# Kernel optimization log

Hardware: AMD Instinct MI355X
Metric: run time of the kernel (lower is better)

The kernel has to match this reference:

```python
import jax, jax.numpy as jnp
import numpy as np

B, T, D = 8, 1024, 512
V = 8192  # codebook_size


def setup_inputs() -> dict:
    key = jax.random.key(0)
    k1, k2, k3 = jax.random.split(key, 3)
    scale_w = float(np.sqrt(2.0 / (D + V)))  # xavier_uniform-ish scale
    scale_c = float(np.sqrt(2.0 / (V + D)))
    return {
        "inputs": jax.random.normal(k1, (B, T, D), dtype=jnp.float32),
        "codebook": jax.random.normal(k2, (V, D), dtype=jnp.float32) * scale_c,
        "W_logits": jax.random.normal(k3, (V, D), dtype=jnp.float32) * scale_w,
        "b_logits": jnp.zeros((V,), dtype=jnp.float32),
    }


def reference(inputs, codebook, W_logits, b_logits):
    # logits = Linear(input_dim -> codebook_size)
    logits = jnp.einsum("btd,vd->btv", inputs, W_logits) + b_logits  # [B,T,V]
    # eval mode: no gumbel noise, no temperature division
    soft_tokens = jax.nn.softmax(logits, axis=-1)
    token_indices = jnp.argmax(soft_tokens, axis=-1)  # [B,T]
    hard_tokens = jax.nn.one_hot(token_indices, codebook.shape[0], dtype=soft_tokens.dtype)
    # straight-through: hard values, soft gradients
    tokens_for_lookup = soft_tokens + jax.lax.stop_gradient(hard_tokens - soft_tokens)
    quantized = jnp.einsum("btv,vd->btd", tokens_for_lookup, codebook)  # [B,T,D]
    commitment_loss = jnp.mean((quantized - jax.lax.stop_gradient(inputs)) ** 2)
    return quantized, token_indices, commitment_loss, soft_tokens, logits
```

## Files before the change

kernel.cpp:

```cpp
#include <hip/hip_runtime.h>
#include <hip/hip_bf16.h>

#define BT_ 8192
#define D_  512
#define V_  8192

#define OFF_Q      0
#define OFF_TOK    4194304
#define OFF_LOSS   4202496
#define OFF_SOFT   4202497
#define OFF_LOGITS 71311361
#define STAGE_F    62922752

#define TAU  0.02f
#define EXP_NEG_TAU 0.98019867f
#define MAXC 64

typedef __attribute__((ext_vector_type(8))) short bf16x8;
typedef __attribute__((ext_vector_type(4))) float f32x4;
typedef __attribute__((ext_vector_type(4))) unsigned short u16x4;

__device__ __forceinline__ unsigned short bf16rne(float f) {
  unsigned int u = __float_as_uint(f);
  return (unsigned short)((u + 0x7fffu + ((u >> 16) & 1u)) >> 16);
}

__global__ __launch_bounds__(256) void to_bf16_k(const f32x4* __restrict__ x,
                                                 const f32x4* __restrict__ w,
                                                 u16x4* __restrict__ xa,
                                                 u16x4* __restrict__ wb) {
  const int n4 = (BT_ * D_) / 4;
  const int half = gridDim.x >> 1;
  const bool isw = blockIdx.x >= half;
  const f32x4* __restrict__ s = isw ? w : x;
  u16x4* __restrict__ d = isw ? wb : xa;
  const int b0 = isw ? blockIdx.x - half : blockIdx.x;
  for (int i = b0 * 256 + threadIdx.x; i < n4; i += half * 256) {
    const f32x4 v = s[i];
    u16x4 o;
    o[0] = bf16rne(v[0]); o[1] = bf16rne(v[1]);
    o[2] = bf16rne(v[2]); o[3] = bf16rne(v[3]);
    d[i] = o;
  }
}

__device__ __forceinline__ void gload_lds16(const void* g, void* l) {
  __builtin_amdgcn_global_load_lds((const __attribute__((address_space(1))) void*)g,
                                   (__attribute__((address_space(3))) void*)l,
                                   16, 0, 0);
}

__device__ __forceinline__ void barf() {
  __builtin_amdgcn_s_barrier();
  asm volatile("" ::: "memory");
}
__device__ __forceinline__ void vmcnt2() { asm volatile("s_waitcnt vmcnt(2)" ::: "memory"); }
__device__ __forceinline__ void vmcnt0() { asm volatile("s_waitcnt vmcnt(0)" ::: "memory"); }

__device__ __forceinline__ void stage_unit(const char* __restrict__ tb, char* ldsRegion,
                                           int ktile, int half, int wid, int lane) {
#pragma unroll
  for (int issue = 0; issue < 2; ++issue) {
    const int d = half * 16384 + issue * 8192 + wid * 1024 + lane * 16;
    const int l = d ^ (((d >> 7) & 7) << 4);
    gload_lds16(tb + (size_t)(l >> 7) * 1024 + ktile * 128 + (l & 127),
                ldsRegion + half * 16384 + issue * 8192 + wid * 1024);
  }
}

__device__ __forceinline__ bf16x8 rdfrag(const char* base, int R, int ks, int g) {
  return *(const bf16x8*)(base + R * 128 + ((ks * 64 + 16 * g) ^ ((R & 7) << 4)));
}

__device__ __forceinline__ void kgroup(int t, int smode, char* lds,
                                       const char* __restrict__ Ab,
                                       const char* __restrict__ Bb,
                                       int wr, int wc, int lane, int wid,
                                       f32x4 (&acc)[8][4]) {
  char* aL = lds + (t & 1) * 32768;
  char* bL = lds + 65536 + (t & 1) * 32768;
  char* aS = lds + ((t & 1) ^ 1) * 32768;
  char* bS = lds + 65536 + ((t & 1) ^ 1) * 32768;
  const int cg = lane & 15, g = lane >> 4;
  bf16x8 a[4][2], b0[2][2], b1[2][2];

#pragma unroll
  for (int m = 0; m < 4; ++m)
#pragma unroll
    for (int ks = 0; ks < 2; ++ks)
      a[m][ks] = rdfrag(aL, wr * 128 + m * 16 + cg, ks, g);
#pragma unroll
  for (int n = 0; n < 2; ++n)
#pragma unroll
    for (int ks = 0; ks < 2; ++ks)
      b0[n][ks] = rdfrag(bL, wc * 64 + n * 16 + cg, ks, g);
  if (smode >= 1) stage_unit(Ab, aS, t + 1, 1, wid, lane);
  barf();
  __builtin_amdgcn_s_setprio(1);
#pragma unroll
  for (int m = 0; m < 4; ++m)
#pragma unroll
    for (int n = 0; n < 2; ++n)
#pragma unroll
      for (int ks = 0; ks < 2; ++ks)
        acc[m][n] = __builtin_amdgcn_mfma_f32_16x16x32_bf16(a[m][ks], b0[n][ks], acc[m][n], 0, 0, 0);
  __builtin_amdgcn_s_setprio(0);
  barf();

#pragma unroll
  for (int n = 0; n < 2; ++n)
#pragma unroll
    for (int ks = 0; ks < 2; ++ks)
      b1[n][ks] = rdfrag(bL, wc * 64 + (n + 2) * 16 + cg, ks, g);
  if (smode >= 1) stage_unit(Bb, bS, t + 1, 0, wid, lane);
  barf();
  __builtin_amdgcn_s_setprio(1);
#pragma unroll
  for (int m = 0; m < 4; ++m)
#pragma unroll
    for (int n = 0; n < 2; ++n)
#pragma unroll
      for (int ks = 0; ks < 2; ++ks)
        acc[m][n + 2] = __builtin_amdgcn_mfma_f32_16x16x32_bf16(a[m][ks], b1[n][ks], acc[m][n + 2], 0, 0, 0);
  __builtin_amdgcn_s_setprio(0);
  barf();

#pragma unroll
  for (int m = 0; m < 4; ++m)
#pragma unroll
    for (int ks = 0; ks < 2; ++ks)
      a[m][ks] = rdfrag(aL, wr * 128 + (m + 4) * 16 + cg, ks, g);
  if (smode >= 1) stage_unit(Bb, bS, t + 1, 1, wid, lane);
  barf();
  __builtin_amdgcn_s_setprio(1);
#pragma unroll
  for (int m = 0; m < 4; ++m)
#pragma unroll
    for (int n = 0; n < 2; ++n)
#pragma unroll
      for (int ks = 0; ks < 2; ++ks)
        acc[m + 4][n + 2] = __builtin_amdgcn_mfma_f32_16x16x32_bf16(a[m][ks], b1[n][ks], acc[m + 4][n + 2], 0, 0, 0);
  __builtin_amdgcn_s_setprio(0);
  barf();

  if (smode == 2) stage_unit(Ab, aL, t + 2, 0, wid, lane);
  barf();
  __builtin_amdgcn_s_setprio(1);
#pragma unroll
  for (int m = 0; m < 4; ++m)
#pragma unroll
    for (int n = 0; n < 2; ++n)
#pragma unroll
      for (int ks = 0; ks < 2; ++ks)
        acc[m + 4][n] = __builtin_amdgcn_mfma_f32_16x16x32_bf16(a[m][ks], b0[n][ks], acc[m + 4][n], 0, 0, 0);
  __builtin_amdgcn_s_setprio(0);
  if (smode == 2) vmcnt2();
  else if (smode == 1) vmcnt0();
  barf();
}

__global__ __launch_bounds__(512) void gemm8(const unsigned short* __restrict__ A,
                                             const unsigned short* __restrict__ B,
                                             const float* __restrict__ bias,
                                             float* __restrict__ C) {
  __shared__ char lds[131072];
  const int tid  = threadIdx.x;
  const int lane = tid & 63;
  const int wid  = tid >> 6;
  const int wr   = wid >> 2, wc = wid & 3;

  const int bid = blockIdx.x;
  const int xcd = bid & 7;
  const int s   = bid >> 3;
  const int by  = (xcd >> 1) * 8 + (s >> 4);
  const int bx  = (xcd & 1) * 16 + (s & 15);
  const int row0 = by * 256, col0 = bx * 256;

  const char* Ab = (const char*)A + (size_t)row0 * (D_ * 2);
  const char* Bb = (const char*)B + (size_t)col0 * (D_ * 2);

  f32x4 acc[8][4] = {};

  stage_unit(Ab, lds, 0, 0, wid, lane);
  stage_unit(Ab, lds, 0, 1, wid, lane);
  stage_unit(Bb, lds + 65536, 0, 0, wid, lane);
  stage_unit(Bb, lds + 65536, 0, 1, wid, lane);
  stage_unit(Ab, lds + 32768, 1, 0, wid, lane);
  vmcnt2();
  barf();

  for (int t = 0; t < 6; ++t)
    kgroup(t, 2, lds, Ab, Bb, wr, wc, lane, wid, acc);
  kgroup(6, 1, lds, Ab, Bb, wr, wc, lane, wid, acc);
  kgroup(7, 0, lds, Ab, Bb, wr, wc, lane, wid, acc);

  const int cg = lane & 15, g = lane >> 4;
  float bv[4];
#pragma unroll
  for (int n = 0; n < 4; ++n) bv[n] = bias[col0 + wc * 64 + n * 16 + cg];

  float* cl = (float*)lds;
  __syncthreads();
#pragma unroll
  for (int h = 0; h < 2; ++h) {
    if (wr == h) {
#pragma unroll
      for (int m = 0; m < 8; ++m)
#pragma unroll
        for (int n = 0; n < 4; ++n) {
          const int cw = ((wc * 64 + n * 16 + cg) + 253) & 255;
#pragma unroll
          for (int rr = 0; rr < 4; ++rr) {
            const int R = m * 16 + 4 * g + rr;
            cl[R * 256 + cw] = acc[m][n][rr] + bv[n];
          }
        }
    }
    __syncthreads();
#pragma unroll
    for (int k = 0; k < 16; ++k) {
      const int r = wid * 16 + k;
      const f32x4 v = *(const f32x4*)((char*)cl + r * 1024 + lane * 16);
      const int grow = row0 + h * 128 + r;
      float* Crow = C + (size_t)grow * V_ + col0;
      if (lane < 63) {
        *((f32x4*)(Crow + 3) + lane) = v;
      } else {
        Crow[255] = v[0]; Crow[0] = v[1]; Crow[1] = v[2]; Crow[2] = v[3];
      }
    }
    __syncthreads();
  }
}

__global__ __launch_bounds__(256) void row_finish(const float* __restrict__ logits,
                                                  const float* __restrict__ xf,
                                                  const float* __restrict__ wf,
                                                  const float* __restrict__ bias,
                                                  float* __restrict__ tokf,
                                                  float* __restrict__ soft) {
  const int row  = blockIdx.x;
  const int tid  = threadIdx.x;
  const int lane = tid & 63;
  const int wv   = tid >> 6;

  __shared__ float redM[4], redS[4];
  __shared__ int   cnum;
  __shared__ int   cidx[MAXC];

  const float* L = logits + (size_t)row * V_;
  float*       S = soft   + (size_t)row * V_;
  const f32x4* L4 = (const f32x4*)(L + 3);
  f32x4*       S4 = (f32x4*)(S + 3);

  f32x4 e[8];
  float m_e = 0.f, s = 0.f;
#pragma unroll
  for (int j = 0; j < 8; ++j) {
    const int i = j * 256 + tid;
    if (i < 2047) {
      const f32x4 v = L4[i];
      f32x4 t;
      t[0] = __expf(v[0]); t[1] = __expf(v[1]);
      t[2] = __expf(v[2]); t[3] = __expf(v[3]);
      e[j] = t;
      m_e = fmaxf(m_e, fmaxf(fmaxf(t[0], t[1]), fmaxf(t[2], t[3])));
      s += t[0] + t[1] + t[2] + t[3];
    } else {
      e[j][0] = 0.f; e[j][1] = 0.f; e[j][2] = 0.f; e[j][3] = 0.f;
    }
  }
  float extra_e = 0.f;
  int   extra_col = -1;
  if (tid < 3)       extra_col = tid;
  else if (tid == 3) extra_col = 8191;
  if (extra_col >= 0) {
    extra_e = __expf(L[extra_col]);
    m_e = fmaxf(m_e, extra_e);
    s += extra_e;
  }
#pragma unroll
  for (int o = 1; o < 64; o <<= 1) {
    m_e = fmaxf(m_e, __shfl_xor(m_e, o));
    s += __shfl_xor(s, o);
  }
  if (lane == 0) { redM[wv] = m_e; redS[wv] = s; }
  if (tid == 0) cnum = 0;
  __syncthreads();
  m_e = fmaxf(fmaxf(redM[0], redM[1]), fmaxf(redM[2], redM[3]));
  s   = redS[0] + redS[1] + redS[2] + redS[3];
  const float si    = 1.0f / s;
  const float thr_e = m_e * EXP_NEG_TAU;

#pragma unroll
  for (int j = 0; j < 8; ++j) {
    const int i = j * 256 + tid;
#pragma unroll
    for (int q = 0; q < 4; ++q)
      if (e[j][q] >= thr_e) {
        const int p = atomicAdd(&cnum, 1);
        if (p < MAXC) cidx[p] = 3 + 4 * i + q;
      }
  }
  if (extra_col >= 0 && extra_e >= thr_e) {
    const int p = atomicAdd(&cnum, 1);
    if (p < MAXC) cidx[p] = extra_col;
  }
  __syncthreads();

  if (wv == 0) {
    const int cnt = min(cnum, MAXC);
    float bestv = -1e30f;
    int   besti = 0x7fffffff;
    const float4* xr4 = (const float4*)(xf + (size_t)row * D_);
    for (int c = 0; c < cnt; ++c) {
      const int col = cidx[c];
      const float4* wr4 = (const float4*)(wf + (size_t)col * D_);
      float p = 0.f;
#pragma unroll
      for (int q = 0; q < 2; ++q) {
        const float4 av = xr4[lane + 64 * q];
        const float4 bvv = wr4[lane + 64 * q];
        p += av.x * bvv.x + av.y * bvv.y + av.z * bvv.z + av.w * bvv.w;
      }
#pragma unroll
      for (int o = 1; o < 64; o <<= 1) p += __shfl_xor(p, o);
      const float tot = p + bias[col];
      if (tot > bestv || (tot == bestv && col < besti)) { bestv = tot; besti = col; }
    }
    if (lane == 0) tokf[row] = (float)besti;
  }

#pragma unroll
  for (int j = 0; j < 8; ++j) {
    const int i = j * 256 + tid;
    if (i < 2047) {
      f32x4 o;
      o[0] = e[j][0] * si; o[1] = e[j][1] * si;
      o[2] = e[j][2] * si; o[3] = e[j][3] * si;
      __builtin_nontemporal_store(o, S4 + i);
    }
  }
  if (extra_col >= 0) S[extra_col] = extra_e * si;
}

__global__ __launch_bounds__(256) void finalize_k(const float* __restrict__ tokf,
                                                  const float* __restrict__ cb,
                                                  const float* __restrict__ xf,
                                                  float* __restrict__ q,
                                                  float* __restrict__ loss) {
  const int row  = blockIdx.x * 4 + (threadIdx.x >> 6);
  const int lane = threadIdx.x & 63;
  const int idx  = (int)tokf[row];
  const f32x4* cr = (const f32x4*)(cb + (size_t)idx * D_);
  const f32x4* xr = (const f32x4*)(xf + (size_t)row * D_);
  f32x4* qr = (f32x4*)(q + (size_t)row * D_);
  float ls = 0.f;
#pragma unroll
  for (int j = 0; j < 2; ++j) {
    const int c = lane + j * 64;
    const f32x4 cv = cr[c];
    const f32x4 xv = xr[c];
    __builtin_nontemporal_store(cv, qr + c);
    const float dx = cv[0] - xv[0], dy = cv[1] - xv[1], dz = cv[2] - xv[2], dw = cv[3] - xv[3];
    ls += dx * dx + dy * dy + dz * dz + dw * dw;
  }
#pragma unroll
  for (int o = 32; o; o >>= 1) ls += __shfl_xor(ls, o);
  if (lane == 0) atomicAdd(loss, ls * (1.0f / 4194304.0f));
}

extern "C" void kernel_launch(void* const* d_in, const int* in_sizes, int n_in,
                              void* d_out, int out_size, void* d_ws, size_t ws_size,
                              hipStream_t stream) {
  const float* x  = (const float*)d_in[0];
  const float* cb = (const float*)d_in[1];
  const float* wl = (const float*)d_in[2];
  const float* bl = (const float*)d_in[3];
  float* out = (float*)d_out;

  float* qout   = out + OFF_Q;
  float* tokf   = out + OFF_TOK;
  float* loss   = out + OFF_LOSS;
  float* soft   = out + OFF_SOFT;
  float* logits = out + OFF_LOGITS;

  unsigned short* Abf = (unsigned short*)(out + STAGE_F);
  unsigned short* Wbf = Abf + (size_t)BT_ * D_;

  hipMemsetAsync(loss, 0, 4, stream);

  to_bf16_k<<<2048, 256, 0, stream>>>((const f32x4*)x, (const f32x4*)wl,
                                      (u16x4*)Abf, (u16x4*)Wbf);
  gemm8<<<1024, 512, 0, stream>>>(Abf, Wbf, bl, logits);
  row_finish<<<8192, 256, 0, stream>>>(logits, x, wl, bl, tokf, soft);
  finalize_k<<<2048, 256, 0, stream>>>(tokf, cb, x, qout, loss);
}
```

Measured before the change: 335.2 us.

## Fuse codebook lookup and commitment loss into row_finish; reverse row order

Moves the quantized codebook gather and squared-error loss accumulation into the row_finish kernel, passing the chosen index through shared memory, which removes the separate finalize kernel launch and its re-read of token indices. Rows are also processed in reverse block order, likely so the most recently written GEMM logits are still cache-resident when read. The cost is an extra block-wide barrier and more atomics to the loss scalar: one per row per wave rather than one per row in a 4-rows-per-block kernel.

```diff
diff --git a/kernel.cpp b/kernel.cpp
--- a/kernel.cpp
+++ b/kernel.cpp
@@ -237,9 +237,12 @@
                                                   const float* __restrict__ xf,
                                                   const float* __restrict__ wf,
                                                   const float* __restrict__ bias,
+                                                  const float* __restrict__ cb,
                                                   float* __restrict__ tokf,
-                                                  float* __restrict__ soft) {
-  const int row  = blockIdx.x;
+                                                  float* __restrict__ soft,
+                                                  float* __restrict__ q,
+                                                  float* __restrict__ loss) {
+  const int row  = (BT_ - 1) - blockIdx.x;
   const int tid  = threadIdx.x;
   const int lane = tid & 63;
   const int wv   = tid >> 6;
@@ -247,6 +250,7 @@
   __shared__ float redM[4], redS[4];
   __shared__ int   cnum;
   __shared__ int   cidx[MAXC];
+  __shared__ int   bestiS;
 
   const float* L = logits + (size_t)row * V_;
   float*       S = soft   + (size_t)row * V_;
@@ -296,10 +300,10 @@
   for (int j = 0; j < 8; ++j) {
     const int i = j * 256 + tid;
 #pragma unroll
-    for (int q = 0; q < 4; ++q)
-      if (e[j][q] >= thr_e) {
+    for (int qq = 0; qq < 4; ++qq)
+      if (e[j][qq] >= thr_e) {
         const int p = atomicAdd(&cnum, 1);
-        if (p < MAXC) cidx[p] = 3 + 4 * i + q;
+        if (p < MAXC) cidx[p] = 3 + 4 * i + qq;
       }
   }
   if (extra_col >= 0 && extra_e >= thr_e) {
@@ -318,9 +322,9 @@
       const float4* wr4 = (const float4*)(wf + (size_t)col * D_);
       float p = 0.f;
 #pragma unroll
-      for (int q = 0; q < 2; ++q) {
-        const float4 av = xr4[lane + 64 * q];
-        const float4 bvv = wr4[lane + 64 * q];
+      for (int qq = 0; qq < 2; ++qq) {
+        const float4 av = xr4[lane + 64 * qq];
+        const float4 bvv = wr4[lane + 64 * qq];
         p += av.x * bvv.x + av.y * bvv.y + av.z * bvv.z + av.w * bvv.w;
       }
 #pragma unroll
@@ -328,7 +332,7 @@
       const float tot = p + bias[col];
       if (tot > bestv || (tot == bestv && col < besti)) { bestv = tot; besti = col; }
     }
-    if (lane == 0) tokf[row] = (float)besti;
+    if (lane == 0) { tokf[row] = (float)besti; bestiS = besti; }
   }
 
 #pragma unroll
@@ -342,32 +346,20 @@
     }
   }
   if (extra_col >= 0) S[extra_col] = extra_e * si;
-}
-
-__global__ __launch_bounds__(256) void finalize_k(const float* __restrict__ tokf,
-                                                  const float* __restrict__ cb,
-                                                  const float* __restrict__ xf,
-                                                  float* __restrict__ q,
-                                                  float* __restrict__ loss) {
-  const int row  = blockIdx.x * 4 + (threadIdx.x >> 6);
-  const int lane = threadIdx.x & 63;
-  const int idx  = (int)tokf[row];
-  const f32x4* cr = (const f32x4*)(cb + (size_t)idx * D_);
-  const f32x4* xr = (const f32x4*)(xf + (size_t)row * D_);
-  f32x4* qr = (f32x4*)(q + (size_t)row * D_);
-  float ls = 0.f;
-#pragma unroll
-  for (int j = 0; j < 2; ++j) {
-    const int c = lane + j * 64;
-    const f32x4 cv = cr[c];
-    const f32x4 xv = xr[c];
-    __builtin_nontemporal_store(cv, qr + c);
-    const float dx = cv[0] - xv[0], dy = cv[1] - xv[1], dz = cv[2] - xv[2], dw = cv[3] - xv[3];
-    ls += dx * dx + dy * dy + dz * dz + dw * dw;
-  }
-#pragma unroll
-  for (int o = 32; o; o >>= 1) ls += __shfl_xor(ls, o);
-  if (lane == 0) atomicAdd(loss, ls * (1.0f / 4194304.0f));
+
+  __syncthreads();
+  const int bi = bestiS;
+  if (tid < 128) {
+    const f32x4 cv = *((const f32x4*)(cb + (size_t)bi * D_) + tid);
+    const f32x4 xv = *((const f32x4*)(xf + (size_t)row * D_) + tid);
+    __builtin_nontemporal_store(cv, (f32x4*)(q + (size_t)row * D_) + tid);
+    const float dx = cv[0] - xv[0], dy = cv[1] - xv[1];
+    const float dz = cv[2] - xv[2], dw = cv[3] - xv[3];
+    float ls = dx * dx + dy * dy + dz * dz + dw * dw;
+#pragma unroll
+    for (int o = 1; o < 64; o <<= 1) ls += __shfl_xor(ls, o);
+    if (lane == 0) atomicAdd(loss, ls * (1.0f / 4194304.0f));
+  }
 }
 
 extern "C" void kernel_launch(void* const* d_in, const int* in_sizes, int n_in,
@@ -393,6 +385,5 @@
   to_bf16_k<<<2048, 256, 0, stream>>>((const f32x4*)x, (const f32x4*)wl,
                                       (u16x4*)Abf, (u16x4*)Wbf);
   gemm8<<<1024, 512, 0, stream>>>(Abf, Wbf, bl, logits);
-  row_finish<<<8192, 256, 0, stream>>>(logits, x, wl, bl, tokf, soft);
-  finalize_k<<<2048, 256, 0, stream>>>(tokf, cb, x, qout, loss);
-}
+  row_finish<<<8192, 256, 0, stream>>>(logits, x, wl, bl, cb, tokf, soft, qout, loss);
+}
```

After: 348.9 us. 4.1% more time.
